# Performance work log

Hardware: AMD Instinct MI355X
Metric: run time of the kernel (lower is better)

The kernel has to match this reference:

```python
import jax, jax.numpy as jnp
import numpy as np

EMBED_DIM = 1024
NUM_HEADS = 16
HEAD_DIM = EMBED_DIM // NUM_HEADS


def setup_inputs() -> dict:
    key = jax.random.key(0)
    k1, k2, k3, k4 = jax.random.split(key, 4)
    B, N, C = 4, 4096, EMBED_DIM
    x = jax.random.normal(k1, (B, N, C), dtype=jnp.float32)
    scale = 1.0 / np.sqrt(C)
    W_qkv = jax.random.normal(k2, (C, 3 * C), dtype=jnp.float32) * scale
    W_out = jax.random.normal(k3, (C, C), dtype=jnp.float32) * scale
    b_out = jax.random.normal(k4, (C,), dtype=jnp.float32) * 0.01
    return {"x": x, "W_qkv": W_qkv, "W_out": W_out, "b_out": b_out}


def reference(x, W_qkv, W_out, b_out):
    B, N, C = x.shape
    H, D = NUM_HEADS, HEAD_DIM
    qkv = (x @ W_qkv).reshape(B, N, 3, H, D)
    qkv = jnp.transpose(qkv, (2, 0, 3, 1, 4))  # (3, B, H, N, D)
    q, k, v = qkv[0], qkv[1], qkv[2]
    q = jax.nn.elu(q) + 1.0
    k = jax.nn.elu(k) + 1.0
    kv = jnp.einsum('bhnd,bhne->bhde', k, v)          # (B,H,D,D)
    num = jnp.einsum('bhnd,bhde->bhne', q, kv)        # (B,H,N,D)
    normalizer = jnp.einsum('bhnd,bhd->bhn', q, k.sum(axis=2))
    out = num / (normalizer[..., None] + 1e-6)
    out = jnp.transpose(out, (0, 2, 1, 3)).reshape(B, N, C)
    return out @ W_out + b_out
```

## Files before the change

### kernel.cpp

```cpp
#include <hip/hip_runtime.h>
#include <hip/hip_bf16.h>

using bf16x8 = __bf16 __attribute__((ext_vector_type(8)));
using f32x4  = float  __attribute__((ext_vector_type(4)));
using u16x8  = unsigned short __attribute__((ext_vector_type(8)));
using u16x4  = unsigned short __attribute__((ext_vector_type(4)));

__device__ __forceinline__ unsigned short f2bf(float f) {
  unsigned u = __builtin_bit_cast(unsigned, f);
  u += 0x7fffu + ((u >> 16) & 1u);
  return (unsigned short)(u >> 16);
}
__device__ __forceinline__ float bf2f(unsigned short h) {
  return __builtin_bit_cast(float, (unsigned)h << 16);
}

__device__ __forceinline__ void gload16(const void* g, void* l) {
  __builtin_amdgcn_global_load_lds(
      (const __attribute__((address_space(1))) void*)g,
      (__attribute__((address_space(3))) void*)l, 16, 0, 0);
}

__device__ __forceinline__ void barrier_raw() {
  asm volatile("" ::: "memory");
  __builtin_amdgcn_s_barrier();
  asm volatile("" ::: "memory");
}
#define LGKM0() asm volatile("s_waitcnt lgkmcnt(0)" ::: "memory")
#define VMC6()  asm volatile("s_waitcnt vmcnt(6)" ::: "memory")
#define VMC0()  asm volatile("s_waitcnt vmcnt(0)" ::: "memory")

__global__ __launch_bounds__(256) void conv_f32_bf16(const float* __restrict__ in,
                                                     unsigned short* __restrict__ out, int n) {
  int stride = gridDim.x * 256 * 4;
  for (int i = (blockIdx.x * 256 + threadIdx.x) * 4; i < n; i += stride) {
    float4 v = *reinterpret_cast<const float4*>(in + i);
    u16x4 o = { f2bf(v.x), f2bf(v.y), f2bf(v.z), f2bf(v.w) };
    *reinterpret_cast<u16x4*>(out + i) = o;
  }
}

__global__ __launch_bounds__(256) void transpose_f32_bf16(const float* __restrict__ in,
                                                          unsigned short* __restrict__ out,
                                                          int R, int C) {
  __shared__ float t[64][65];
  int c0 = blockIdx.x * 64, r0 = blockIdx.y * 64;
  int lx = threadIdx.x & 63, ly = threadIdx.x >> 6;
#pragma unroll
  for (int i = 0; i < 16; ++i) {
    int r = ly * 16 + i;
    t[r][lx] = in[(size_t)(r0 + r) * C + c0 + lx];
  }
  __syncthreads();
#pragma unroll
  for (int i = 0; i < 16; ++i) {
    int c = ly * 16 + i;
    out[(size_t)(c0 + c) * R + r0 + lx] = f2bf(t[lx][c]);
  }
}

__device__ __forceinline__ void gemm256_mainloop(
    const unsigned short* __restrict__ A, const unsigned short* __restrict__ Bt,
    int brow, int bcol, char* lds, f32x4 (&acc)[8][4]) {
  constexpr int NT = 16;
  const int tid  = threadIdx.x;
  const int lane = tid & 63;
  const int w    = tid >> 6;
  const int wr   = w >> 2, wc = w & 3;
  const int lr   = lane & 15, kg = lane >> 4;

  const int o0 = tid * 16;
  const int o1 = 8192 + tid * 16;
  const int p0 = o0 ^ (((o0 >> 7) & 7) << 4);
  const int p1 = o1 ^ (((o1 >> 7) & 7) << 4);
  const int off0 = (p0 >> 7) * 2048 + (p0 & 127);
  const int off1 = (p1 >> 7) * 2048 + (p1 & 127);
  const int wq = w << 10;

  const int xr  = (lr & 7) << 4;
  const int ck0 = (kg * 16) ^ xr;
  const int ck1 = (64 + kg * 16) ^ xr;
  const int aoff = wr * 16384 + lr * 128;
  const int boff = 32768 + (wc >> 1) * 16384 + (wc & 1) * 8192 + lr * 128;

  auto STAGE = [&](const unsigned short* G, int rowbase, int t, int region) {
    const char* gb = (const char*)(G + (size_t)rowbase * 1024 + t * 64);
    char* lb = lds + region + wq;
    gload16(gb + off0, lb);
    gload16(gb + off1, lb + 8192);
  };

  STAGE(Bt, bcol,       0, 32768);
  STAGE(Bt, bcol + 128, 0, 32768 + 16384);
  STAGE(A,  brow,       0, 0);
  STAGE(A,  brow + 128, 0, 16384);
  STAGE(Bt, bcol,       1, 65536 + 32768);
  STAGE(Bt, bcol + 128, 1, 65536 + 32768 + 16384);
  STAGE(A,  brow,       1, 65536);
  VMC6();
  barrier_raw();

  bf16x8 aF[4][2], bF[4][2];
  for (int t = 0; t < NT; ++t) {
    const int bufo  = (t & 1) << 16;
    const int nbufo = bufo ^ 65536;
    const char* LA = lds + bufo + aoff;
    const char* LB = lds + bufo + boff;

#pragma unroll
    for (int n = 0; n < 4; ++n) {
      bF[n][0] = __builtin_bit_cast(bf16x8, *(const u16x8*)(LB + n * 2048 + ck0));
      bF[n][1] = __builtin_bit_cast(bf16x8, *(const u16x8*)(LB + n * 2048 + ck1));
    }
#pragma unroll
    for (int m = 0; m < 4; ++m) {
      aF[m][0] = __builtin_bit_cast(bf16x8, *(const u16x8*)(LA + m * 2048 + ck0));
      aF[m][1] = __builtin_bit_cast(bf16x8, *(const u16x8*)(LA + m * 2048 + ck1));
    }
    if (t + 1 < NT) STAGE(A, brow + 128, t + 1, nbufo + 16384);
    barrier_raw();
    LGKM0();
    __builtin_amdgcn_s_setprio(1);
#pragma unroll
    for (int m = 0; m < 4; ++m)
#pragma unroll
      for (int n = 0; n < 2; ++n) {
        acc[m][n] = __builtin_amdgcn_mfma_f32_16x16x32_bf16(aF[m][0], bF[n][0], acc[m][n], 0, 0, 0);
        acc[m][n] = __builtin_amdgcn_mfma_f32_16x16x32_bf16(aF[m][1], bF[n][1], acc[m][n], 0, 0, 0);
      }
    __builtin_amdgcn_s_setprio(0);
    barrier_raw();

    if (t + 2 < NT) STAGE(Bt, bcol, t + 2, bufo + 32768);
    barrier_raw();
    __builtin_amdgcn_s_setprio(1);
#pragma unroll
    for (int m = 0; m < 4; ++m)
#pragma unroll
      for (int n = 2; n < 4; ++n) {
        acc[m][n] = __builtin_amdgcn_mfma_f32_16x16x32_bf16(aF[m][0], bF[n][0], acc[m][n], 0, 0, 0);
        acc[m][n] = __builtin_amdgcn_mfma_f32_16x16x32_bf16(aF[m][1], bF[n][1], acc[m][n], 0, 0, 0);
      }
    __builtin_amdgcn_s_setprio(0);
    barrier_raw();

#pragma unroll
    for (int m = 0; m < 4; ++m) {
      aF[m][0] = __builtin_bit_cast(bf16x8, *(const u16x8*)(LA + (m + 4) * 2048 + ck0));
      aF[m][1] = __builtin_bit_cast(bf16x8, *(const u16x8*)(LA + (m + 4) * 2048 + ck1));
    }
    if (t + 2 < NT) STAGE(Bt, bcol + 128, t + 2, bufo + 32768 + 16384);
    barrier_raw();
    LGKM0();
    __builtin_amdgcn_s_setprio(1);
#pragma unroll
    for (int m = 0; m < 4; ++m)
#pragma unroll
      for (int n = 2; n < 4; ++n) {
        acc[m + 4][n] = __builtin_amdgcn_mfma_f32_16x16x32_bf16(aF[m][0], bF[n][0], acc[m + 4][n], 0, 0, 0);
        acc[m + 4][n] = __builtin_amdgcn_mfma_f32_16x16x32_bf16(aF[m][1], bF[n][1], acc[m + 4][n], 0, 0, 0);
      }
    __builtin_amdgcn_s_setprio(0);
    barrier_raw();

    if (t + 2 < NT) STAGE(A, brow, t + 2, bufo);
    barrier_raw();
    __builtin_amdgcn_s_setprio(1);
#pragma unroll
    for (int m = 0; m < 4; ++m)
#pragma unroll
      for (int n = 0; n < 2; ++n) {
        acc[m + 4][n] = __builtin_amdgcn_mfma_f32_16x16x32_bf16(aF[m][0], bF[n][0], acc[m + 4][n], 0, 0, 0);
        acc[m + 4][n] = __builtin_amdgcn_mfma_f32_16x16x32_bf16(aF[m][1], bF[n][1], acc[m + 4][n], 0, 0, 0);
      }
    __builtin_amdgcn_s_setprio(0);
    if (t + 2 < NT) { VMC6(); } else { VMC0(); }
    barrier_raw();
  }
}

__global__ __launch_bounds__(512, 2) void gemm_qkv(
    const unsigned short* __restrict__ xbf, const unsigned short* __restrict__ wt,
    unsigned short* __restrict__ q, unsigned short* __restrict__ k, unsigned short* __restrict__ v) {
  __shared__ __align__(16) char lds[131072];
  f32x4 acc[8][4] = {};
  const int bid = blockIdx.x;
  const int swz = (bid & 7) * 96 + (bid >> 3);
  const int tn = swz / 64, tm = swz % 64;
  const int brow = tm * 256, bcol = tn * 256;
  gemm256_mainloop(xbf, wt, brow, bcol, lds, acc);

  const int lane = threadIdx.x & 63, w = threadIdx.x >> 6;
  const int wr = w >> 2, wc = w & 3;
  const int lr = lane & 15, kg = lane >> 4;
#pragma unroll
  for (int m = 0; m < 8; ++m)
#pragma unroll
    for (int n = 0; n < 4; ++n)
#pragma unroll
      for (int r = 0; r < 4; ++r) {
        int grow = brow + wr * 128 + m * 16 + kg * 4 + r;
        int gcol = bcol + wc * 64 + n * 16 + lr;
        float val = acc[m][n][r];
        int tt = gcol >> 10;
        int h = (gcol >> 6) & 15;
        int d = gcol & 63;
        int b = grow >> 12, s = grow & 4095;
        size_t idx = ((size_t)(b * 16 + h) * 4096 + s) * 64 + d;
        if (tt < 2) {
          val = val > 0.f ? val + 1.f : __expf(val);
          (tt == 0 ? q : k)[idx] = f2bf(val);
        } else {
          v[idx] = f2bf(val);
        }
      }
}

__global__ __launch_bounds__(512, 2) void gemm_out(
    const unsigned short* __restrict__ attn, const unsigned short* __restrict__ wt,
    const float* __restrict__ bias, float* __restrict__ out) {
  __shared__ __align__(16) char lds[131072];
  f32x4 acc[8][4] = {};
  const int bid = blockIdx.x;
  const int swz = (bid & 7) * 32 + (bid >> 3);
  const int tn = swz >> 6, tm = swz & 63;
  const int brow = tm * 256, bcol = tn * 256;
  gemm256_mainloop(attn, wt, brow, bcol, lds, acc);

  const int lane = threadIdx.x & 63, w = threadIdx.x >> 6;
  const int wr = w >> 2, wc = w & 3;
  const int lr = lane & 15, kg = lane >> 4;
#pragma unroll
  for (int m = 0; m < 8; ++m)
#pragma unroll
    for (int n = 0; n < 4; ++n)
#pragma unroll
      for (int r = 0; r < 4; ++r) {
        int grow = brow + wr * 128 + m * 16 + kg * 4 + r;
        int gcol = bcol + wc * 64 + n * 16 + lr;
        out[(size_t)grow * 1024 + gcol] = acc[m][n][r] + bias[gcol];
      }
}

__global__ __launch_bounds__(256) void kv_kernel(
    const unsigned short* __restrict__ k, const unsigned short* __restrict__ v,
    float* __restrict__ kv, float* __restrict__ ksum) {
  const int bid = blockIdx.x;
  const int bh = bid >> 3, chunk = bid & 7;
  const unsigned short* kb = k + (size_t)bh * 4096 * 64 + chunk * 512 * 64;
  const unsigned short* vb = v + (size_t)bh * 4096 * 64 + chunk * 512 * 64;
  __shared__ unsigned short ks[64 * 64];
  __shared__ unsigned short vs[64 * 64];
  const int tid = threadIdx.x;
  const int ty = tid >> 4, tx = tid & 15;
  float acc[4][4] = {};
  float ksacc[4] = {};
  for (int t = 0; t < 8; ++t) {
    const unsigned short* ksrc = kb + t * 4096;
    const unsigned short* vsrc = vb + t * 4096;
    *reinterpret_cast<u16x8*>(&ks[tid * 8])        = *reinterpret_cast<const u16x8*>(ksrc + tid * 8);
    *reinterpret_cast<u16x8*>(&ks[2048 + tid * 8]) = *reinterpret_cast<const u16x8*>(ksrc + 2048 + tid * 8);
    *reinterpret_cast<u16x8*>(&vs[tid * 8])        = *reinterpret_cast<const u16x8*>(vsrc + tid * 8);
    *reinterpret_cast<u16x8*>(&vs[2048 + tid * 8]) = *reinterpret_cast<const u16x8*>(vsrc + 2048 + tid * 8);
    __syncthreads();
#pragma unroll 4
    for (int nn = 0; nn < 64; ++nn) {
      u16x4 ku = *reinterpret_cast<const u16x4*>(&ks[nn * 64 + ty * 4]);
      u16x4 vu = *reinterpret_cast<const u16x4*>(&vs[nn * 64 + tx * 4]);
      float kd[4], ve[4];
#pragma unroll
      for (int i = 0; i < 4; ++i) { kd[i] = bf2f(ku[i]); ve[i] = bf2f(vu[i]); }
#pragma unroll
      for (int i = 0; i < 4; ++i) ksacc[i] += kd[i];
#pragma unroll
      for (int i = 0; i < 4; ++i)
#pragma unroll
        for (int j = 0; j < 4; ++j) acc[i][j] += kd[i] * ve[j];
    }
    __syncthreads();
  }
  float* kvb = kv + (size_t)bh * 4096;
#pragma unroll
  for (int i = 0; i < 4; ++i)
#pragma unroll
    for (int j = 0; j < 4; ++j)
      atomicAdd(&kvb[(tx * 4 + j) * 64 + ty * 4 + i], acc[i][j]);
  if (tx == 0) {
#pragma unroll
    for (int i = 0; i < 4; ++i) atomicAdd(&ksum[bh * 64 + ty * 4 + i], ksacc[i]);
  }
}

__global__ __launch_bounds__(256) void num_kernel(
    const unsigned short* __restrict__ q, const float* __restrict__ kv,
    const float* __restrict__ ksum, unsigned short* __restrict__ attn) {
  const int bid = blockIdx.x;
  const int bh = bid >> 6, sblk = bid & 63;
  const int b = bh >> 4, h = bh & 15;
  __shared__ unsigned short kvs[64 * 72];
  __shared__ float ksum_s[64];
  __shared__ float norm_s[64];
  const int tid = threadIdx.x;
  const float* kvb = kv + (size_t)bh * 4096;
#pragma unroll
  for (int r = 0; r < 4; ++r) {
    int e = r * 1024 + tid * 4;
    float4 f = *reinterpret_cast<const float4*>(&kvb[e]);
    int row = e >> 6, col = e & 63;
    u16x4 o = { f2bf(f.x), f2bf(f.y), f2bf(f.z), f2bf(f.w) };
    *reinterpret_cast<u16x4*>(&kvs[row * 72 + col]) = o;
  }
  if (tid < 16) {
    float4 f = *reinterpret_cast<const float4*>(&ksum[bh * 64 + tid * 4]);
    ksum_s[tid * 4 + 0] = f.x; ksum_s[tid * 4 + 1] = f.y;
    ksum_s[tid * 4 + 2] = f.z; ksum_s[tid * 4 + 3] = f.w;
  }
  __syncthreads();

  const int lane = tid & 63, w = tid >> 6;
  const int lr = lane & 15, kg = lane >> 4;
  const int s0 = sblk * 64 + w * 16;
  const unsigned short* qrow = q + ((size_t)bh * 4096 + s0 + lr) * 64 + kg * 8;
  u16x8 a0u = *reinterpret_cast<const u16x8*>(qrow);
  u16x8 a1u = *reinterpret_cast<const u16x8*>(qrow + 32);
  bf16x8 a0 = __builtin_bit_cast(bf16x8, a0u);
  bf16x8 a1 = __builtin_bit_cast(bf16x8, a1u);

  float p = 0.f;
#pragma unroll
  for (int j = 0; j < 8; ++j) {
    p += bf2f(a0u[j]) * ksum_s[kg * 8 + j];
    p += bf2f(a1u[j]) * ksum_s[32 + kg * 8 + j];
  }
  p += __shfl_xor(p, 16);
  p += __shfl_xor(p, 32);
  if (kg == 0) norm_s[w * 16 + lr] = p;

  f32x4 accs[4];
#pragma unroll
  for (int jf = 0; jf < 4; ++jf) {
    u16x8 b0u = *reinterpret_cast<const u16x8*>(&kvs[(jf * 16 + lr) * 72 + kg * 8]);
    u16x8 b1u = *reinterpret_cast<const u16x8*>(&kvs[(jf * 16 + lr) * 72 + 32 + kg * 8]);
    f32x4 c = {0.f, 0.f, 0.f, 0.f};
    c = __builtin_amdgcn_mfma_f32_16x16x32_bf16(a0, __builtin_bit_cast(bf16x8, b0u), c, 0, 0, 0);
    c = __builtin_amdgcn_mfma_f32_16x16x32_bf16(a1, __builtin_bit_cast(bf16x8, b1u), c, 0, 0, 0);
    accs[jf] = c;
  }
  float dn[4];
#pragma unroll
  for (int r = 0; r < 4; ++r) dn[r] = norm_s[w * 16 + kg * 4 + r] + 1e-6f;

  unsigned short* ab = attn + (size_t)b * 4096 * 1024 + h * 64;
#pragma unroll
  for (int jf = 0; jf < 4; ++jf)
#pragma unroll
    for (int r = 0; r < 4; ++r) {
      int s = s0 + kg * 4 + r;
      int e2 = jf * 16 + lr;
      ab[(size_t)s * 1024 + e2] = f2bf(accs[jf][r] / dn[r]);
    }
}

extern "C" void kernel_launch(void* const* d_in, const int* in_sizes, int n_in,
                              void* d_out, int out_size, void* d_ws, size_t ws_size,
                              hipStream_t stream) {
  const float* x     = (const float*)d_in[0];
  const float* W_qkv = (const float*)d_in[1];
  const float* W_out = (const float*)d_in[2];
  const float* b_out = (const float*)d_in[3];
  float* out = (float*)d_out;

  unsigned short* xbf   = (unsigned short*)d_ws;
  unsigned short* attnb = xbf;
  unsigned short* wqkvT = xbf + 16777216;
  unsigned short* woutT = wqkvT + 3145728;
  unsigned short* qb    = woutT + 1048576;
  unsigned short* kb    = qb + 16777216;
  unsigned short* vb    = kb + 16777216;
  float* kvw            = (float*)(vb + 16777216);
  float* ksumw          = kvw + 262144;

  conv_f32_bf16<<<2048, 256, 0, stream>>>(x, xbf, 16777216);
  transpose_f32_bf16<<<dim3(48, 16), 256, 0, stream>>>(W_qkv, wqkvT, 1024, 3072);
  transpose_f32_bf16<<<dim3(16, 16), 256, 0, stream>>>(W_out, woutT, 1024, 1024);
  hipMemsetAsync(kvw, 0, (262144 + 4096) * sizeof(float), stream);
  gemm_qkv<<<768, 512, 0, stream>>>(xbf, wqkvT, qb, kb, vb);
  kv_kernel<<<512, 256, 0, stream>>>(kb, vb, kvw, ksumw);
  num_kernel<<<4096, 256, 0, stream>>>(qb, kvw, ksumw, attnb);
  gemm_out<<<256, 512, 0, stream>>>(attnb, woutT, b_out, out);
}
```

Measured before the change: 268.8 us.

## Split B fragment loads, reorder MFMA k-loop, and remap block tile swizzle

Each tile iteration now loads B fragments in two halves, the second half just before the MFMAs that use it, and the MFMA loops are reordered so the k index is outermost. This cuts register pressure and interleaves independent accumulators. The global->LDS staging of the next B tile moves later in the iteration and is paired with the A stage. Block-to-tile mapping in both GEMMs changes to a grouped swizzle of 8 row tiles per XCD chunk, aiming for better L2 reuse. The later B staging must not overwrite LDS that is still being read, which depends on the double-buffer offsets staying correct.

```diff
diff --git a/kernel.cpp b/kernel.cpp
--- a/kernel.cpp
+++ b/kernel.cpp
@@ -108,7 +108,7 @@
     const char* LB = lds + bufo + boff;
 
 #pragma unroll
-    for (int n = 0; n < 4; ++n) {
+    for (int n = 0; n < 2; ++n) {
       bF[n][0] = __builtin_bit_cast(bf16x8, *(const u16x8*)(LB + n * 2048 + ck0));
       bF[n][1] = __builtin_bit_cast(bf16x8, *(const u16x8*)(LB + n * 2048 + ck1));
     }
@@ -122,25 +122,30 @@
     LGKM0();
     __builtin_amdgcn_s_setprio(1);
 #pragma unroll
-    for (int m = 0; m < 4; ++m)
-#pragma unroll
-      for (int n = 0; n < 2; ++n) {
-        acc[m][n] = __builtin_amdgcn_mfma_f32_16x16x32_bf16(aF[m][0], bF[n][0], acc[m][n], 0, 0, 0);
-        acc[m][n] = __builtin_amdgcn_mfma_f32_16x16x32_bf16(aF[m][1], bF[n][1], acc[m][n], 0, 0, 0);
-      }
+    for (int kk = 0; kk < 2; ++kk)
+#pragma unroll
+      for (int m = 0; m < 4; ++m)
+#pragma unroll
+        for (int n = 0; n < 2; ++n)
+          acc[m][n] = __builtin_amdgcn_mfma_f32_16x16x32_bf16(aF[m][kk], bF[n][kk], acc[m][n], 0, 0, 0);
     __builtin_amdgcn_s_setprio(0);
     barrier_raw();
 
-    if (t + 2 < NT) STAGE(Bt, bcol, t + 2, bufo + 32768);
-    barrier_raw();
+#pragma unroll
+    for (int n = 2; n < 4; ++n) {
+      bF[n][0] = __builtin_bit_cast(bf16x8, *(const u16x8*)(LB + n * 2048 + ck0));
+      bF[n][1] = __builtin_bit_cast(bf16x8, *(const u16x8*)(LB + n * 2048 + ck1));
+    }
+    barrier_raw();
+    LGKM0();
     __builtin_amdgcn_s_setprio(1);
 #pragma unroll
-    for (int m = 0; m < 4; ++m)
-#pragma unroll
-      for (int n = 2; n < 4; ++n) {
-        acc[m][n] = __builtin_amdgcn_mfma_f32_16x16x32_bf16(aF[m][0], bF[n][0], acc[m][n], 0, 0, 0);
-        acc[m][n] = __builtin_amdgcn_mfma_f32_16x16x32_bf16(aF[m][1], bF[n][1], acc[m][n], 0, 0, 0);
-      }
+    for (int kk = 0; kk < 2; ++kk)
+#pragma unroll
+      for (int m = 0; m < 4; ++m)
+#pragma unroll
+        for (int n = 2; n < 4; ++n)
+          acc[m][n] = __builtin_amdgcn_mfma_f32_16x16x32_bf16(aF[m][kk], bF[n][kk], acc[m][n], 0, 0, 0);
     __builtin_amdgcn_s_setprio(0);
     barrier_raw();
 
@@ -149,30 +154,33 @@
       aF[m][0] = __builtin_bit_cast(bf16x8, *(const u16x8*)(LA + (m + 4) * 2048 + ck0));
       aF[m][1] = __builtin_bit_cast(bf16x8, *(const u16x8*)(LA + (m + 4) * 2048 + ck1));
     }
-    if (t + 2 < NT) STAGE(Bt, bcol + 128, t + 2, bufo + 32768 + 16384);
+    if (t + 2 < NT) STAGE(Bt, bcol, t + 2, bufo + 32768);
     barrier_raw();
     LGKM0();
     __builtin_amdgcn_s_setprio(1);
 #pragma unroll
-    for (int m = 0; m < 4; ++m)
-#pragma unroll
-      for (int n = 2; n < 4; ++n) {
-        acc[m + 4][n] = __builtin_amdgcn_mfma_f32_16x16x32_bf16(aF[m][0], bF[n][0], acc[m + 4][n], 0, 0, 0);
-        acc[m + 4][n] = __builtin_amdgcn_mfma_f32_16x16x32_bf16(aF[m][1], bF[n][1], acc[m + 4][n], 0, 0, 0);
-      }
+    for (int kk = 0; kk < 2; ++kk)
+#pragma unroll
+      for (int m = 0; m < 4; ++m)
+#pragma unroll
+        for (int n = 2; n < 4; ++n)
+          acc[m + 4][n] = __builtin_amdgcn_mfma_f32_16x16x32_bf16(aF[m][kk], bF[n][kk], acc[m + 4][n], 0, 0, 0);
     __builtin_amdgcn_s_setprio(0);
     barrier_raw();
 
-    if (t + 2 < NT) STAGE(A, brow, t + 2, bufo);
+    if (t + 2 < NT) {
+      STAGE(Bt, bcol + 128, t + 2, bufo + 32768 + 16384);
+      STAGE(A,  brow,       t + 2, bufo);
+    }
     barrier_raw();
     __builtin_amdgcn_s_setprio(1);
 #pragma unroll
-    for (int m = 0; m < 4; ++m)
-#pragma unroll
-      for (int n = 0; n < 2; ++n) {
-        acc[m + 4][n] = __builtin_amdgcn_mfma_f32_16x16x32_bf16(aF[m][0], bF[n][0], acc[m + 4][n], 0, 0, 0);
-        acc[m + 4][n] = __builtin_amdgcn_mfma_f32_16x16x32_bf16(aF[m][1], bF[n][1], acc[m + 4][n], 0, 0, 0);
-      }
+    for (int kk = 0; kk < 2; ++kk)
+#pragma unroll
+      for (int m = 0; m < 4; ++m)
+#pragma unroll
+        for (int n = 0; n < 2; ++n)
+          acc[m + 4][n] = __builtin_amdgcn_mfma_f32_16x16x32_bf16(aF[m][kk], bF[n][kk], acc[m + 4][n], 0, 0, 0);
     __builtin_amdgcn_s_setprio(0);
     if (t + 2 < NT) { VMC6(); } else { VMC0(); }
     barrier_raw();
@@ -185,8 +193,9 @@
   __shared__ __align__(16) char lds[131072];
   f32x4 acc[8][4] = {};
   const int bid = blockIdx.x;
-  const int swz = (bid & 7) * 96 + (bid >> 3);
-  const int tn = swz / 64, tm = swz % 64;
+  const int r = bid & 7, i = bid >> 3;
+  const int tm = r * 8 + (i & 7);
+  const int tn = i >> 3;
   const int brow = tm * 256, bcol = tn * 256;
   gemm256_mainloop(xbf, wt, brow, bcol, lds, acc);
 
@@ -198,10 +207,10 @@
 #pragma unroll
     for (int n = 0; n < 4; ++n)
 #pragma unroll
-      for (int r = 0; r < 4; ++r) {
-        int grow = brow + wr * 128 + m * 16 + kg * 4 + r;
+      for (int rr = 0; rr < 4; ++rr) {
+        int grow = brow + wr * 128 + m * 16 + kg * 4 + rr;
         int gcol = bcol + wc * 64 + n * 16 + lr;
-        float val = acc[m][n][r];
+        float val = acc[m][n][rr];
         int tt = gcol >> 10;
         int h = (gcol >> 6) & 15;
         int d = gcol & 63;
@@ -222,8 +231,9 @@
   __shared__ __align__(16) char lds[131072];
   f32x4 acc[8][4] = {};
   const int bid = blockIdx.x;
-  const int swz = (bid & 7) * 32 + (bid >> 3);
-  const int tn = swz >> 6, tm = swz & 63;
+  const int r = bid & 7, i = bid >> 3;
+  const int tm = r * 8 + (i & 7);
+  const int tn = i >> 3;
   const int brow = tm * 256, bcol = tn * 256;
   gemm256_mainloop(attn, wt, brow, bcol, lds, acc);
 
@@ -235,10 +245,10 @@
 #pragma unroll
     for (int n = 0; n < 4; ++n)
 #pragma unroll
-      for (int r = 0; r < 4; ++r) {
-        int grow = brow + wr * 128 + m * 16 + kg * 4 + r;
+      for (int rr = 0; rr < 4; ++rr) {
+        int grow = brow + wr * 128 + m * 16 + kg * 4 + rr;
         int gcol = bcol + wc * 64 + n * 16 + lr;
-        out[(size_t)grow * 1024 + gcol] = acc[m][n][r] + bias[gcol];
+        out[(size_t)grow * 1024 + gcol] = acc[m][n][rr] + bias[gcol];
       }
 }
 
```

New measurement: 261.2 us. 1.03x faster.
